# Kernel optimization log

Hardware: AMD Instinct MI355X
Metric: run time of the kernel (lower is better)

## Reference

```python
import jax, jax.numpy as jnp
import numpy as np

N = 50000      # nodes
E = 800000     # edges (before self loops)
IN = 128       # in_channels
C = 64         # out_channels per head
H = 4          # heads (both layers)
NEG_SLOPE = 0.2


def setup_inputs():
    key = jax.random.key(0)
    ks = jax.random.split(key, 14)
    nrm = lambda k, sh, s: jax.random.normal(k, sh, dtype=jnp.float32) * s
    x = nrm(ks[0], (N, IN), 1.0)
    edge_index = jax.random.randint(ks[1], (2, E), 0, N, dtype=jnp.int32)
    batch = jnp.zeros((N,), dtype=jnp.int32)
    edge_attr = jax.random.uniform(ks[2], (E, 1), dtype=jnp.float32)
    # layer 1 params (PyG GATConv: lin, att_src, att_dst, lin_edge, att_edge, bias)
    W1 = nrm(ks[3], (IN, H * C), 1.0 / np.sqrt(IN))
    We1 = nrm(ks[4], (1, H * C), 1.0)
    att_s1 = nrm(ks[5], (H, C), 1.0 / np.sqrt(C))
    att_d1 = nrm(ks[6], (H, C), 1.0 / np.sqrt(C))
    att_e1 = nrm(ks[7], (H, C), 1.0 / np.sqrt(C))
    b1 = jnp.zeros((H * C,), dtype=jnp.float32)
    # layer 2 params (in = H*C = 256)
    W2 = nrm(ks[8], (H * C, H * C), 1.0 / np.sqrt(H * C))
    We2 = nrm(ks[9], (1, H * C), 1.0)
    att_s2 = nrm(ks[10], (H, C), 1.0 / np.sqrt(C))
    att_d2 = nrm(ks[11], (H, C), 1.0 / np.sqrt(C))
    att_e2 = nrm(ks[12], (H, C), 1.0 / np.sqrt(C))
    b2 = jnp.zeros((H * C,), dtype=jnp.float32)
    return dict(x=x, edge_index=edge_index, batch=batch, edge_attr=edge_attr,
                W1=W1, We1=We1, att_s1=att_s1, att_d1=att_d1, att_e1=att_e1, b1=b1,
                W2=W2, We2=We2, att_s2=att_s2, att_d2=att_d2, att_e2=att_e2, b2=b2)


def gat_layer(h_in, src, dst, e_attr, W, We, att_s, att_d, att_e, b):
    n = h_in.shape[0]
    h = (h_in @ W).reshape(n, H, C)                      # [N,H,C]
    a_src = jnp.einsum('nhc,hc->nh', h, att_s)           # [N,H]
    a_dst = jnp.einsum('nhc,hc->nh', h, att_d)
    e = (e_attr @ We).reshape(-1, H, C)                  # [E',H,C]
    a_edge = jnp.einsum('ehc,hc->eh', e, att_e)          # [E',H]
    alpha = jax.nn.leaky_relu(a_src[src] + a_dst[dst] + a_edge, NEG_SLOPE)
    # softmax over edges grouped by destination node
    amax = jax.ops.segment_max(alpha, dst, num_segments=n)
    amax = jnp.where(jnp.isfinite(amax), amax, 0.0)
    ex = jnp.exp(alpha - amax[dst])
    denom = jax.ops.segment_sum(ex, dst, num_segments=n)
    a = ex / (denom[dst] + 1e-16)                        # [E',H]
    out = jax.ops.segment_sum(a[:, :, None] * h[src], dst, num_segments=n)
    return out.reshape(n, H * C) + b


def reference(x, edge_index, batch, edge_attr,
              W1, We1, att_s1, att_d1, att_e1, b1,
              W2, We2, att_s2, att_d2, att_e2, b2):
    n = x.shape[0]
    # PyG GATConv default: add self loops, self-loop edge_attr = mean fill
    loop = jnp.arange(n, dtype=edge_index.dtype)
    src = jnp.concatenate([edge_index[0], loop])
    dst = jnp.concatenate([edge_index[1], loop])
    ea_fill = jnp.broadcast_to(edge_attr.mean(axis=0, keepdims=True), (n, edge_attr.shape[1]))
    ea = jnp.concatenate([edge_attr, ea_fill], axis=0)
    h1 = gat_layer(x, src, dst, ea, W1, We1, att_s1, att_d1, att_e1, b1)
    h2 = gat_layer(h1, src, dst, ea, W2, We2, att_s2, att_d2, att_e2, b2)
    return h2
```

## Files before the change

### kernel.cpp

```cpp
#include <hip/hip_runtime.h>

#define NEG_SLOPE 0.2f

typedef __attribute__((ext_vector_type(8))) short bf16x8;
typedef __attribute__((ext_vector_type(4))) float f32x4;

__device__ inline unsigned short f2bf(float x) {
  unsigned int u = __float_as_uint(x);
  u += 0x7fffu + ((u >> 16) & 1u);
  return (unsigned short)(u >> 16);
}

__device__ inline unsigned fkey(float x) {
  unsigned u = __float_as_uint(x);
  return (u >> 31) ? ~u : (u | 0x80000000u);
}
__device__ inline float fkey_dec(unsigned k) {
  unsigned u = (k & 0x80000000u) ? (k ^ 0x80000000u) : ~k;
  return __uint_as_float(u);
}


__global__ void hist_kernel(const int* __restrict__ ei, int* __restrict__ counts,
                            int E, int Etot) {
  int e = blockIdx.x * blockDim.x + threadIdx.x;
  if (e >= Etot) return;
  int d = (e < E) ? ei[E + e] : (e - E);
  atomicAdd(&counts[d], 1);
}

__global__ void mean_kernel(const float* __restrict__ ea, float* __restrict__ acc, int E) {
  int i = blockIdx.x * blockDim.x + threadIdx.x;
  float s = 0.f;
  for (; i < E; i += gridDim.x * blockDim.x) s += ea[i];
#pragma unroll
  for (int off = 1; off < 64; off <<= 1) s += __shfl_xor(s, off, 64);
  if ((threadIdx.x & 63) == 0) atomicAdd(acc, s);
}

__global__ void scan_blocksum(const int* __restrict__ counts, int* __restrict__ bsum, int Nn) {
  int base = blockIdx.x * 4096 + threadIdx.x * 16;
  int s = 0;
#pragma unroll
  for (int i = 0; i < 16; i++) { int idx = base + i; if (idx < Nn) s += counts[idx]; }
#pragma unroll
  for (int off = 1; off < 64; off <<= 1) s += __shfl_xor(s, off, 64);
  __shared__ int ws_[4];
  if ((threadIdx.x & 63) == 0) ws_[threadIdx.x >> 6] = s;
  __syncthreads();
  if (threadIdx.x == 0) bsum[blockIdx.x] = ws_[0] + ws_[1] + ws_[2] + ws_[3];
}

__global__ void scan_offsets(int* bsum, int nb, int* rowptrN,
                             const float* meanacc, float* meanv, int E) {
  if (threadIdx.x == 0 && blockIdx.x == 0) {
    int acc = 0;
    for (int i = 0; i < nb; i++) { int v = bsum[i]; bsum[i] = acc; acc += v; }
    *rowptrN = acc;
    *meanv = *meanacc / (float)E;
  }
}

__global__ void scan_final(const int* __restrict__ counts, const int* __restrict__ bsum,
                           int* __restrict__ rowptr, int* __restrict__ cursor, int Nn) {
  int base = blockIdx.x * 4096 + threadIdx.x * 16;
  int v[16]; int s = 0;
#pragma unroll
  for (int i = 0; i < 16; i++) { int idx = base + i; v[i] = (idx < Nn) ? counts[idx] : 0; s += v[i]; }
  int lane = threadIdx.x & 63, wv = threadIdx.x >> 6;
  int incl = s;
#pragma unroll
  for (int off = 1; off < 64; off <<= 1) {
    int y = __shfl_up(incl, off, 64);
    if (lane >= off) incl += y;
  }
  __shared__ int wtot[4];
  if (lane == 63) wtot[wv] = incl;
  __syncthreads();
  int run = bsum[blockIdx.x] + incl - s;
  for (int i = 0; i < wv; i++) run += wtot[i];
  for (int i = 0; i < 16; i++) {
    int idx = base + i;
    if (idx < Nn) { rowptr[idx] = run; cursor[idx] = run; }
    run += v[i];
  }
}

__global__ void scatter_kernel(const int* __restrict__ ei, const float* __restrict__ eattr,
                               const float* __restrict__ meanv,
                               int* __restrict__ cursor, int2* __restrict__ epack,
                               int E, int Etot) {
  int e = blockIdx.x * blockDim.x + threadIdx.x;
  if (e >= Etot) return;
  int d, s; float ea;
  if (e < E) { d = ei[E + e]; s = ei[e]; ea = eattr[e]; }
  else       { d = e - E;     s = e - E; ea = meanv[0]; }
  int pos = atomicAdd(&cursor[d], 1);
  epack[pos] = make_int2(s, __float_as_int(ea));
}

__global__ void weatt_kernel(const float* __restrict__ We1, const float* __restrict__ atte1,
                             const float* __restrict__ We2, const float* __restrict__ atte2,
                             float* __restrict__ weatt1, float* __restrict__ weatt2) {
  int t = threadIdx.x;
  const float* We = (t < 256) ? We1 : We2;
  const float* at = (t < 256) ? atte1 : atte2;
  float* wo = (t < 256) ? weatt1 : weatt2;
  int i = t & 255;
  float p = We[i] * at[i];
#pragma unroll
  for (int off = 1; off < 64; off <<= 1) p += __shfl_xor(p, off, 64);
  if ((i & 63) == 0) wo[i >> 6] = p;
}

__global__ void wtrans_kernel(const float* __restrict__ W1, unsigned short* __restrict__ Wt1,
                              const float* __restrict__ W2, unsigned short* __restrict__ Wt2) {
  int b = blockIdx.x;
  const float* W; unsigned short* Wt; int K, t;
  if (b < 128) { W = W1; Wt = Wt1; K = 128; t = b * 256 + threadIdx.x; }
  else         { W = W2; Wt = Wt2; K = 256; t = (b - 128) * 256 + threadIdx.x; }
  int n = t & 255, k = t >> 8;
  if (k >= K) return;
  Wt[(size_t)n * K + k] = f2bf(W[(size_t)k * 256 + n]);
}


template <int AF32>
__global__ __launch_bounds__(512) void gemm_att(const void* __restrict__ Ain,
                                                const unsigned short* __restrict__ Wt,
                                                unsigned short* __restrict__ Hb,
                                                const float* __restrict__ atts,
                                                const float* __restrict__ attd,
                                                float* __restrict__ asrc,
                                                float* __restrict__ adst,
                                                unsigned* __restrict__ gmaxk,
                                                int M, int K) {
  __shared__ short As[128 * 64];
  __shared__ short Bs[256 * 64];
  const int tid = threadIdx.x;
  const int lane = tid & 63, wv = tid >> 6;
  const int wm = wv >> 2, wn = wv & 3;
  const int l15 = lane & 15, l4 = lane >> 4;
  const int bm = blockIdx.x * 128;

  f32x4 acc[4][4] = {};

  for (int k0 = 0; k0 < K; k0 += 64) {
    {
      int r0 = tid >> 3, kc = (tid & 7) * 8;
#pragma unroll
      for (int rr = 0; rr < 2; rr++) {
        int r = r0 + rr * 64;
        int gr = bm + r;
        bf16x8 v = {};
        if (gr < M) {
          if (AF32) {
            const float* src = (const float*)Ain + (size_t)gr * K + k0 + kc;
            float4 f0 = *(const float4*)src;
            float4 f1 = *(const float4*)(src + 4);
            v[0] = (short)f2bf(f0.x); v[1] = (short)f2bf(f0.y);
            v[2] = (short)f2bf(f0.z); v[3] = (short)f2bf(f0.w);
            v[4] = (short)f2bf(f1.x); v[5] = (short)f2bf(f1.y);
            v[6] = (short)f2bf(f1.z); v[7] = (short)f2bf(f1.w);
          } else {
            v = *(const bf16x8*)((const unsigned short*)Ain + (size_t)gr * K + k0 + kc);
          }
        }
        *(bf16x8*)&As[(r * 64 + kc) ^ ((r & 7) << 3)] = v;
      }
    }
    {
      int c = tid & 7, nb = tid >> 3;
#pragma unroll
      for (int it = 0; it < 4; it++) {
        int n = nb + 64 * it;
        bf16x8 v = *(const bf16x8*)&Wt[(size_t)n * K + k0 + c * 8];
        *(bf16x8*)&Bs[(n * 64 + c * 8) ^ ((n & 7) << 3)] = v;
      }
    }
    __syncthreads();
    bf16x8 af[4][2], bfr[4][2];
#pragma unroll
    for (int rt = 0; rt < 4; rt++)
#pragma unroll
      for (int ks = 0; ks < 2; ks++) {
        int row = wm * 64 + rt * 16 + l15;
        int kb = l4 * 8 + ks * 32;
        af[rt][ks] = *(const bf16x8*)&As[(row * 64 + kb) ^ ((row & 7) << 3)];
      }
#pragma unroll
    for (int ct = 0; ct < 4; ct++)
#pragma unroll
      for (int ks = 0; ks < 2; ks++) {
        int n = wn * 64 + ct * 16 + l15;
        int kb = l4 * 8 + ks * 32;
        bfr[ct][ks] = *(const bf16x8*)&Bs[(n * 64 + kb) ^ ((n & 7) << 3)];
      }
#pragma unroll
    for (int rt = 0; rt < 4; rt++)
#pragma unroll
      for (int ct = 0; ct < 4; ct++)
#pragma unroll
        for (int ks = 0; ks < 2; ks++)
          acc[rt][ct] = __builtin_amdgcn_mfma_f32_16x16x32_bf16(
              af[rt][ks], bfr[ct][ks], acc[rt][ct], 0, 0, 0);
    __syncthreads();
  }

  float s_att[4], d_att[4];
#pragma unroll
  for (int ct = 0; ct < 4; ct++) {
    s_att[ct] = atts[wn * 64 + ct * 16 + l15];
    d_att[ct] = attd[wn * 64 + ct * 16 + l15];
  }
  float ps[4][4] = {}, pd[4][4] = {};
#pragma unroll
  for (int rt = 0; rt < 4; rt++)
#pragma unroll
    for (int ct = 0; ct < 4; ct++)
#pragma unroll
      for (int i = 0; i < 4; i++) {
        float v = acc[rt][ct][i];
        int gr = bm + wm * 64 + rt * 16 + l4 * 4 + i;
        if (gr < M) Hb[(size_t)gr * 256 + wn * 64 + ct * 16 + l15] = f2bf(v);
        ps[rt][i] = fmaf(v, s_att[ct], ps[rt][i]);
        pd[rt][i] = fmaf(v, d_att[ct], pd[rt][i]);
      }
#pragma unroll
  for (int rt = 0; rt < 4; rt++)
#pragma unroll
    for (int i = 0; i < 4; i++) {
#pragma unroll
      for (int off = 1; off < 16; off <<= 1) {
        ps[rt][i] += __shfl_xor(ps[rt][i], off, 64);
        pd[rt][i] += __shfl_xor(pd[rt][i], off, 64);
      }
    }
  float mx = ps[0][0];
#pragma unroll
  for (int rt = 0; rt < 4; rt++)
#pragma unroll
    for (int i = 0; i < 4; i++) mx = fmaxf(mx, ps[rt][i]);
  mx = fmaxf(mx, __shfl_xor(mx, 16, 64));
  mx = fmaxf(mx, __shfl_xor(mx, 32, 64));
  if (lane == 0) atomicMax(&gmaxk[wn * 32], fkey(mx));
  if (l15 == 0) {
#pragma unroll
    for (int rt = 0; rt < 4; rt++)
#pragma unroll
      for (int i = 0; i < 4; i++) {
        int gr = bm + wm * 64 + rt * 16 + l4 * 4 + i;
        if (gr < M) {
          asrc[gr * 4 + wn] = ps[rt][i];
          adst[gr * 4 + wn] = pd[rt][i];
        }
      }
  }
}


template <int OUTBF>
__global__ __launch_bounds__(256) void gat_agg(const unsigned short* __restrict__ Hb,
                                               const float* __restrict__ asrc,
                                               const float* __restrict__ adst,
                                               const int* __restrict__ rowptr,
                                               const int2* __restrict__ epack,
                                               const float* __restrict__ weatt,
                                               const unsigned* __restrict__ gmaxk,
                                               const float* __restrict__ bias,
                                               unsigned short* __restrict__ outb,
                                               float* __restrict__ outf, int Nn) {
  int wid = (blockIdx.x * blockDim.x + threadIdx.x) >> 6;
  int lane = threadIdx.x & 63;
  if (wid >= Nn) return;
  int beg = rowptr[wid], end = rowptr[wid + 1];
  int hh = lane >> 4;
  float wa = weatt[hh];
  float ad = adst[wid * 4 + hh];
  float braw = ad + fkey_dec(gmaxk[hh * 32]) + fmaxf(wa, 0.f);
  float b = fmaxf(braw, NEG_SLOPE * braw);
  unsigned co = (unsigned)lane * 4u;

  float s0 = 0.f, s1 = 0.f;
  float4 a0 = {0.f, 0.f, 0.f, 0.f}, a1 = {0.f, 0.f, 0.f, 0.f};
  int p = beg;
  for (; p + 1 < end; p += 2) {
    int2 e0 = epack[p], e1 = epack[p + 1];
    float al0 = fmaf(__int_as_float(e0.y), wa, asrc[e0.x * 4 + hh] + ad);
    float al1 = fmaf(__int_as_float(e1.y), wa, asrc[e1.x * 4 + hh] + ad);
    al0 = fmaxf(al0, NEG_SLOPE * al0);
    al1 = fmaxf(al1, NEG_SLOPE * al1);
    uint2 hv0 = *(const uint2*)&Hb[(size_t)((unsigned)e0.x * 256u + co)];
    uint2 hv1 = *(const uint2*)&Hb[(size_t)((unsigned)e1.x * 256u + co)];
    float w0 = __expf(al0 - b);
    float w1 = __expf(al1 - b);
    s0 += w0;
    s1 += w1;
    a0.x = fmaf(w0, __uint_as_float(hv0.x << 16), a0.x);
    a0.y = fmaf(w0, __uint_as_float(hv0.x & 0xffff0000u), a0.y);
    a0.z = fmaf(w0, __uint_as_float(hv0.y << 16), a0.z);
    a0.w = fmaf(w0, __uint_as_float(hv0.y & 0xffff0000u), a0.w);
    a1.x = fmaf(w1, __uint_as_float(hv1.x << 16), a1.x);
    a1.y = fmaf(w1, __uint_as_float(hv1.x & 0xffff0000u), a1.y);
    a1.z = fmaf(w1, __uint_as_float(hv1.y << 16), a1.z);
    a1.w = fmaf(w1, __uint_as_float(hv1.y & 0xffff0000u), a1.w);
  }
  if (p < end) {
    int2 e0 = epack[p];
    float al0 = fmaf(__int_as_float(e0.y), wa, asrc[e0.x * 4 + hh] + ad);
    al0 = fmaxf(al0, NEG_SLOPE * al0);
    uint2 hv0 = *(const uint2*)&Hb[(size_t)((unsigned)e0.x * 256u + co)];
    float w0 = __expf(al0 - b);
    s0 += w0;
    a0.x = fmaf(w0, __uint_as_float(hv0.x << 16), a0.x);
    a0.y = fmaf(w0, __uint_as_float(hv0.x & 0xffff0000u), a0.y);
    a0.z = fmaf(w0, __uint_as_float(hv0.y << 16), a0.z);
    a0.w = fmaf(w0, __uint_as_float(hv0.y & 0xffff0000u), a0.w);
  }
  float inv = 1.f / (s0 + s1 + 1e-16f);
  float4 b4 = *(const float4*)&bias[co];
  float4 r;
  r.x = fmaf(a0.x + a1.x, inv, b4.x);
  r.y = fmaf(a0.y + a1.y, inv, b4.y);
  r.z = fmaf(a0.z + a1.z, inv, b4.z);
  r.w = fmaf(a0.w + a1.w, inv, b4.w);
  if (OUTBF) {
    unsigned lo = (unsigned)f2bf(r.x) | ((unsigned)f2bf(r.y) << 16);
    unsigned hi = (unsigned)f2bf(r.z) | ((unsigned)f2bf(r.w) << 16);
    *(uint2*)&outb[(size_t)wid * 256 + co] = make_uint2(lo, hi);
  } else {
    *(float4*)&outf[(size_t)wid * 256 + co] = r;
  }
}


extern "C" void kernel_launch(void* const* d_in, const int* in_sizes, int n_in,
                              void* d_out, int out_size, void* d_ws, size_t ws_size,
                              hipStream_t stream) {
  (void)n_in; (void)out_size; (void)ws_size;
  const float* x     = (const float*)d_in[0];
  const int*   ei    = (const int*)d_in[1];
  const float* eattr = (const float*)d_in[3];
  const float* W1    = (const float*)d_in[4];
  const float* We1   = (const float*)d_in[5];
  const float* atts1 = (const float*)d_in[6];
  const float* attd1 = (const float*)d_in[7];
  const float* atte1 = (const float*)d_in[8];
  const float* b1    = (const float*)d_in[9];
  const float* W2    = (const float*)d_in[10];
  const float* We2   = (const float*)d_in[11];
  const float* atts2 = (const float*)d_in[12];
  const float* attd2 = (const float*)d_in[13];
  const float* atte2 = (const float*)d_in[14];
  const float* b2    = (const float*)d_in[15];
  float* out = (float*)d_out;

  const int Nn   = in_sizes[0] / 128;
  const int E    = in_sizes[1] / 2;
  const int Etot = E + Nn;

  char* p = (char*)d_ws;
  auto alloc = [&](size_t bytes) { void* r = (void*)p; p += (bytes + 255) & ~(size_t)255; return r; };
  int*      counts  = (int*)alloc((size_t)Nn * 4);
  float*    meanacc = (float*)alloc(4);
  unsigned* gmaxk1  = (unsigned*)alloc(512);
  unsigned* gmaxk2  = (unsigned*)alloc(512);
  char* zero_end = p;
  int*   rowptr  = (int*)alloc((size_t)(Nn + 1) * 4);
  int*   cursor  = (int*)alloc((size_t)Nn * 4);
  int2*  epack   = (int2*)alloc((size_t)Etot * 8);
  int*   bsum    = (int*)alloc(64 * 4);
  float* meanv   = (float*)alloc(4);
  float* weatt1  = (float*)alloc(16);
  float* weatt2  = (float*)alloc(16);
  float* asrc    = (float*)alloc((size_t)Nn * 4 * 4);
  float* adst    = (float*)alloc((size_t)Nn * 4 * 4);
  unsigned short* hbuf = (unsigned short*)alloc((size_t)Nn * 256 * 2);
  unsigned short* h1b  = (unsigned short*)alloc((size_t)Nn * 256 * 2);
  unsigned short* Wt1  = (unsigned short*)alloc((size_t)256 * 128 * 2);
  unsigned short* Wt2  = (unsigned short*)alloc((size_t)256 * 256 * 2);

  const int NB = (Nn + 4095) / 4096;

  hipMemsetAsync(counts, 0, (size_t)(zero_end - (char*)counts), stream);

  hist_kernel<<<(Etot + 255) / 256, 256, 0, stream>>>(ei, counts, E, Etot);
  mean_kernel<<<512, 256, 0, stream>>>(eattr, meanacc, E);
  scan_blocksum<<<NB, 256, 0, stream>>>(counts, bsum, Nn);
  scan_offsets<<<1, 64, 0, stream>>>(bsum, NB, rowptr + Nn, meanacc, meanv, E);
  scan_final<<<NB, 256, 0, stream>>>(counts, bsum, rowptr, cursor, Nn);
  scatter_kernel<<<(Etot + 255) / 256, 256, 0, stream>>>(ei, eattr, meanv, cursor, epack, E, Etot);
  weatt_kernel<<<1, 512, 0, stream>>>(We1, atte1, We2, atte2, weatt1, weatt2);
  wtrans_kernel<<<384, 256, 0, stream>>>(W1, Wt1, W2, Wt2);

  const int gemmBlocks = (Nn + 127) / 128;
  const int nodeBlocks = (Nn + 3) / 4;

  gemm_att<1><<<gemmBlocks, 512, 0, stream>>>(x, Wt1, hbuf, atts1, attd1,
                                              asrc, adst, gmaxk1, Nn, 128);
  gat_agg<1><<<nodeBlocks, 256, 0, stream>>>(hbuf, asrc, adst, rowptr, epack,
                                             weatt1, gmaxk1, b1, h1b, nullptr, Nn);
  gemm_att<0><<<gemmBlocks, 512, 0, stream>>>(h1b, Wt2, hbuf, atts2, attd2,
                                              asrc, adst, gmaxk2, Nn, 256);
  gat_agg<0><<<nodeBlocks, 256, 0, stream>>>(hbuf, asrc, adst, rowptr, epack,
                                             weatt2, gmaxk2, b2, nullptr, out, Nn);
}
```

Measured before the change: 350.2 us.

## Compute edge attention weights cooperatively per 16 lanes and fuse histogram with mean

Result: slower. 459.2 us (+31.1%).

```diff
diff --git a/kernel.cpp b/kernel.cpp
--- a/kernel.cpp
+++ b/kernel.cpp
@@ -21,21 +21,19 @@
 }
 
 
-__global__ void hist_kernel(const int* __restrict__ ei, int* __restrict__ counts,
-                            int E, int Etot) {
+__global__ void hist_mean_kernel(const int* __restrict__ ei, const float* __restrict__ eattr,
+                                 int* __restrict__ counts, float* __restrict__ acc,
+                                 int E, int Etot) {
   int e = blockIdx.x * blockDim.x + threadIdx.x;
-  if (e >= Etot) return;
-  int d = (e < E) ? ei[E + e] : (e - E);
-  atomicAdd(&counts[d], 1);
-}
-
-__global__ void mean_kernel(const float* __restrict__ ea, float* __restrict__ acc, int E) {
-  int i = blockIdx.x * blockDim.x + threadIdx.x;
   float s = 0.f;
-  for (; i < E; i += gridDim.x * blockDim.x) s += ea[i];
+  if (e < Etot) {
+    int d = (e < E) ? ei[E + e] : (e - E);
+    atomicAdd(&counts[d], 1);
+    if (e < E) s = eattr[e];
+  }
 #pragma unroll
   for (int off = 1; off < 64; off <<= 1) s += __shfl_xor(s, off, 64);
-  if ((threadIdx.x & 63) == 0) atomicAdd(acc, s);
+  if ((threadIdx.x & 63) == 0 && s != 0.f) atomicAdd(acc, s);
 }
 
 __global__ void scan_blocksum(const int* __restrict__ counts, int* __restrict__ bsum, int Nn) {
@@ -259,6 +257,29 @@
 }
 
 
+#define AGG_PH1(CNT)                                                        \
+  int src = 0; float w = 0.f;                                               \
+  if (il < (CNT)) {                                                         \
+    int2 e = epack[p + il];                                                 \
+    float al = fmaf(__int_as_float(e.y), wa, asrc[e.x * 4 + hh] + ad);      \
+    al = fmaxf(al, NEG_SLOPE * al);                                         \
+    w = __expf(al - b);                                                     \
+    src = e.x;                                                              \
+  }                                                                         \
+  ssum += w;
+
+#define AGG_GATHER(i)                                                       \
+  {                                                                         \
+    int sl = (i) | hb16;                                                    \
+    int si = __shfl(src, sl, 64);                                           \
+    float wi = __shfl(w, sl, 64);                                           \
+    uint2 hv = *(const uint2*)&Hb[(size_t)((unsigned)si * 256u + co)];      \
+    acc.x = fmaf(wi, __uint_as_float(hv.x << 16), acc.x);                   \
+    acc.y = fmaf(wi, __uint_as_float(hv.x & 0xffff0000u), acc.y);           \
+    acc.z = fmaf(wi, __uint_as_float(hv.y << 16), acc.z);                   \
+    acc.w = fmaf(wi, __uint_as_float(hv.y & 0xffff0000u), acc.w);           \
+  }
+
 template <int OUTBF>
 __global__ __launch_bounds__(256) void gat_agg(const unsigned short* __restrict__ Hb,
                                                const float* __restrict__ asrc,
@@ -275,55 +296,39 @@
   if (wid >= Nn) return;
   int beg = rowptr[wid], end = rowptr[wid + 1];
   int hh = lane >> 4;
+  int il = lane & 15;
+  int hb16 = lane & 48;
   float wa = weatt[hh];
   float ad = adst[wid * 4 + hh];
   float braw = ad + fkey_dec(gmaxk[hh * 32]) + fmaxf(wa, 0.f);
   float b = fmaxf(braw, NEG_SLOPE * braw);
   unsigned co = (unsigned)lane * 4u;
 
-  float s0 = 0.f, s1 = 0.f;
-  float4 a0 = {0.f, 0.f, 0.f, 0.f}, a1 = {0.f, 0.f, 0.f, 0.f};
+  float ssum = 0.f;
+  float4 acc = {0.f, 0.f, 0.f, 0.f};
+
   int p = beg;
-  for (; p + 1 < end; p += 2) {
-    int2 e0 = epack[p], e1 = epack[p + 1];
-    float al0 = fmaf(__int_as_float(e0.y), wa, asrc[e0.x * 4 + hh] + ad);
-    float al1 = fmaf(__int_as_float(e1.y), wa, asrc[e1.x * 4 + hh] + ad);
-    al0 = fmaxf(al0, NEG_SLOPE * al0);
-    al1 = fmaxf(al1, NEG_SLOPE * al1);
-    uint2 hv0 = *(const uint2*)&Hb[(size_t)((unsigned)e0.x * 256u + co)];
-    uint2 hv1 = *(const uint2*)&Hb[(size_t)((unsigned)e1.x * 256u + co)];
-    float w0 = __expf(al0 - b);
-    float w1 = __expf(al1 - b);
-    s0 += w0;
-    s1 += w1;
-    a0.x = fmaf(w0, __uint_as_float(hv0.x << 16), a0.x);
-    a0.y = fmaf(w0, __uint_as_float(hv0.x & 0xffff0000u), a0.y);
-    a0.z = fmaf(w0, __uint_as_float(hv0.y << 16), a0.z);
-    a0.w = fmaf(w0, __uint_as_float(hv0.y & 0xffff0000u), a0.w);
-    a1.x = fmaf(w1, __uint_as_float(hv1.x << 16), a1.x);
-    a1.y = fmaf(w1, __uint_as_float(hv1.x & 0xffff0000u), a1.y);
-    a1.z = fmaf(w1, __uint_as_float(hv1.y << 16), a1.z);
-    a1.w = fmaf(w1, __uint_as_float(hv1.y & 0xffff0000u), a1.w);
-  }
-  if (p < end) {
-    int2 e0 = epack[p];
-    float al0 = fmaf(__int_as_float(e0.y), wa, asrc[e0.x * 4 + hh] + ad);
-    al0 = fmaxf(al0, NEG_SLOPE * al0);
-    uint2 hv0 = *(const uint2*)&Hb[(size_t)((unsigned)e0.x * 256u + co)];
-    float w0 = __expf(al0 - b);
-    s0 += w0;
-    a0.x = fmaf(w0, __uint_as_float(hv0.x << 16), a0.x);
-    a0.y = fmaf(w0, __uint_as_float(hv0.x & 0xffff0000u), a0.y);
-    a0.z = fmaf(w0, __uint_as_float(hv0.y << 16), a0.z);
-    a0.w = fmaf(w0, __uint_as_float(hv0.y & 0xffff0000u), a0.w);
-  }
-  float inv = 1.f / (s0 + s1 + 1e-16f);
+  for (; p + 16 <= end; p += 16) {
+    AGG_PH1(16)
+#pragma unroll
+    for (int i = 0; i < 16; i++) AGG_GATHER(i)
+  }
+  int cnt = end - p;
+  if (cnt > 0) {
+    AGG_PH1(cnt)
+    for (int i = 0; i < cnt; i++) AGG_GATHER(i)
+  }
+
+#pragma unroll
+  for (int off = 1; off < 16; off <<= 1) ssum += __shfl_xor(ssum, off, 64);
+
+  float inv = 1.f / (ssum + 1e-16f);
   float4 b4 = *(const float4*)&bias[co];
   float4 r;
-  r.x = fmaf(a0.x + a1.x, inv, b4.x);
-  r.y = fmaf(a0.y + a1.y, inv, b4.y);
-  r.z = fmaf(a0.z + a1.z, inv, b4.z);
-  r.w = fmaf(a0.w + a1.w, inv, b4.w);
+  r.x = fmaf(acc.x, inv, b4.x);
+  r.y = fmaf(acc.y, inv, b4.y);
+  r.z = fmaf(acc.z, inv, b4.z);
+  r.w = fmaf(acc.w, inv, b4.w);
   if (OUTBF) {
     unsigned lo = (unsigned)f2bf(r.x) | ((unsigned)f2bf(r.y) << 16);
     unsigned hi = (unsigned)f2bf(r.z) | ((unsigned)f2bf(r.w) << 16);
@@ -384,8 +389,7 @@
 
   hipMemsetAsync(counts, 0, (size_t)(zero_end - (char*)counts), stream);
 
-  hist_kernel<<<(Etot + 255) / 256, 256, 0, stream>>>(ei, counts, E, Etot);
-  mean_kernel<<<512, 256, 0, stream>>>(eattr, meanacc, E);
+  hist_mean_kernel<<<(Etot + 255) / 256, 256, 0, stream>>>(ei, eattr, counts, meanacc, E, Etot);
   scan_blocksum<<<NB, 256, 0, stream>>>(counts, bsum, Nn);
   scan_offsets<<<1, 64, 0, stream>>>(bsum, NB, rowptr + Nn, meanacc, meanv, E);
   scan_final<<<NB, 256, 0, stream>>>(counts, bsum, rowptr, cursor, Nn);
```
